# Performance work log

Measured on AMD Instinct MI355X. Metric: run time of the kernel, lower is better.

The kernel has to match this reference:

```python
import jax, jax.numpy as jnp
import numpy as np

SMOOTHING = 0.05
CONFIDENCE = 1.0 - SMOOTHING
B, C = 32768, 2048


def setup_inputs() -> dict:
    key = jax.random.key(0)
    k1, k2, k3 = jax.random.split(key, 3)
    x = jax.random.normal(k1, (B, C), dtype=jnp.float32)
    target = jax.random.randint(k2, (B,), 0, C, dtype=jnp.int64)
    class_loss_weight = jax.random.uniform(k3, (C,), dtype=jnp.float32)
    return {"x": x, "target": target, "class_loss_weight": class_loss_weight}


def reference(x, target, class_loss_weight):
    # logprobs: [B, C]
    logprobs = jax.nn.log_softmax(x, axis=-1)
    # nll_loss: [B] = -logprobs[i, target[i]]
    nll_loss = -jnp.take_along_axis(logprobs, target[:, None], axis=-1)[:, 0]
    # smooth_loss: [B] = -mean over classes
    smooth_loss = -jnp.mean(logprobs, axis=-1)
    # per-sample class weights (vectorized replacement for the python loop)
    w = class_loss_weight[target]  # [B]
    w_sum = jnp.sum(w)
    loss = CONFIDENCE * nll_loss * w + SMOOTHING * smooth_loss
    return jnp.sum(loss) / w_sum
```

## Files before the change

### kernel.cpp

```cpp
#include <hip/hip_runtime.h>
#include <math.h>

#define SMOOTHING_F   0.05f
#define CONFIDENCE_F  0.95f
#define C_DIM         2048

#define STAGE1_BLOCKS 128

__global__ __launch_bounds__(256) void ls_main(
    const float* __restrict__ x,
    const int*   __restrict__ target,
    const float* __restrict__ cw,
    double*      __restrict__ ws)
{
    const int row  = blockIdx.x;
    const int tid  = threadIdx.x;
    const int lane = tid & 63;
    const int wave = tid >> 6;

    const int t = target[row];

    const float4* xr = (const float4*)(x + (size_t)row * C_DIM);
    const float4 a = xr[tid];
    const float4 b = xr[tid + 256];

    const float wt = cw[t];
    const float xt = x[(size_t)row * C_DIM + t];

    float se = __expf(a.x) + __expf(a.y) + __expf(a.z) + __expf(a.w)
             + __expf(b.x) + __expf(b.y) + __expf(b.z) + __expf(b.w);
    float sx = (a.x + a.y) + (a.z + a.w) + (b.x + b.y) + (b.z + b.w);

#pragma unroll
    for (int off = 32; off > 0; off >>= 1) {
        se += __shfl_xor(se, off, 64);
        sx += __shfl_xor(sx, off, 64);
    }

    __shared__ float sSe[4], sSx[4];
    if (lane == 0) { sSe[wave] = se; sSx[wave] = sx; }
    __syncthreads();
    if (tid == 0) {
        const float seT = (sSe[0] + sSe[1]) + (sSe[2] + sSe[3]);
        const float sxT = (sSx[0] + sSx[1]) + (sSx[2] + sSx[3]);
        const float lse = __logf(seT);
        const float nll    = lse - xt;
        const float smooth = lse - sxT * (1.0f / C_DIM);
        const double loss = (double)(CONFIDENCE_F * nll * wt + SMOOTHING_F * smooth);
        ws[2 * (size_t)row]     = loss;
        ws[2 * (size_t)row + 1] = (double)wt;
    }
}

__global__ __launch_bounds__(256) void ls_reduce1(
    const double* __restrict__ ws, double* __restrict__ out1, int B)
{
    const int tid  = threadIdx.x;
    const int lane = tid & 63;
    const int wave = tid >> 6;

    double L = 0.0, W = 0.0;
    for (int i = blockIdx.x * 256 + tid; i < B; i += STAGE1_BLOCKS * 256) {
        L += ws[2 * (size_t)i];
        W += ws[2 * (size_t)i + 1];
    }
#pragma unroll
    for (int off = 32; off > 0; off >>= 1) {
        L += __shfl_xor(L, off, 64);
        W += __shfl_xor(W, off, 64);
    }
    __shared__ double sL[4], sW[4];
    if (lane == 0) { sL[wave] = L; sW[wave] = W; }
    __syncthreads();
    if (tid == 0) {
        out1[2 * blockIdx.x]     = (sL[0] + sL[1]) + (sL[2] + sL[3]);
        out1[2 * blockIdx.x + 1] = (sW[0] + sW[1]) + (sW[2] + sW[3]);
    }
}

__global__ __launch_bounds__(128) void ls_reduce2(
    const double* __restrict__ in1, float* __restrict__ out)
{
    const int tid  = threadIdx.x;
    const int lane = tid & 63;
    const int wave = tid >> 6;

    double L = in1[2 * tid];
    double W = in1[2 * tid + 1];
#pragma unroll
    for (int off = 32; off > 0; off >>= 1) {
        L += __shfl_xor(L, off, 64);
        W += __shfl_xor(W, off, 64);
    }
    __shared__ double sL[2], sW[2];
    if (lane == 0) { sL[wave] = L; sW[wave] = W; }
    __syncthreads();
    if (tid == 0) out[0] = (float)((sL[0] + sL[1]) / (sW[0] + sW[1]));
}

extern "C" void kernel_launch(void* const* d_in, const int* in_sizes, int n_in,
                              void* d_out, int out_size, void* d_ws, size_t ws_size,
                              hipStream_t stream) {
    const float* x      = (const float*)d_in[0];
    const int*   target = (const int*)  d_in[1];
    const float* cw     = (const float*)d_in[2];
    float*       out    = (float*)d_out;
    double*      ws     = (double*)d_ws;

    const int B = in_sizes[1];
    double* stage1 = ws + 2 * (size_t)B;

    ls_main<<<B, 256, 0, stream>>>(x, target, cw, ws);
    ls_reduce1<<<STAGE1_BLOCKS, 256, 0, stream>>>(ws, stage1, B);
    ls_reduce2<<<1, 128, 0, stream>>>(stage1, out);
}
```

Baseline: 351.1 us.

## Use nontemporal loads/stores and collapse two-stage reduction into one kernel

The main kernel now loads x with nontemporal loads, writes each row's loss and weight pair as a single nontemporal 16-byte store, and declares a launch-bounds occupancy hint. The two-kernel reduction is replaced by one 1024-thread single-block kernel that reads the paired partials as vectors. This removes one kernel launch and its inter-kernel gap, at the cost of the final reduction running on a single CU over 32K pairs.

```diff
diff --git a/kernel.cpp b/kernel.cpp
--- a/kernel.cpp
+++ b/kernel.cpp
@@ -5,9 +5,10 @@
 #define CONFIDENCE_F  0.95f
 #define C_DIM         2048
 
-#define STAGE1_BLOCKS 128
+typedef float  f32x4 __attribute__((ext_vector_type(4)));
+typedef double f64x2 __attribute__((ext_vector_type(2)));
 
-__global__ __launch_bounds__(256) void ls_main(
+__global__ __launch_bounds__(256, 8) void ls_main(
     const float* __restrict__ x,
     const int*   __restrict__ target,
     const float* __restrict__ cw,
@@ -20,9 +21,9 @@
 
     const int t = target[row];
 
-    const float4* xr = (const float4*)(x + (size_t)row * C_DIM);
-    const float4 a = xr[tid];
-    const float4 b = xr[tid + 256];
+    const f32x4* xr = (const f32x4*)(x + (size_t)row * C_DIM);
+    const f32x4 a = __builtin_nontemporal_load(&xr[tid]);
+    const f32x4 b = __builtin_nontemporal_load(&xr[tid + 256]);
 
     const float wt = cw[t];
     const float xt = x[(size_t)row * C_DIM + t];
@@ -46,56 +47,40 @@
         const float lse = __logf(seT);
         const float nll    = lse - xt;
         const float smooth = lse - sxT * (1.0f / C_DIM);
-        const double loss = (double)(CONFIDENCE_F * nll * wt + SMOOTHING_F * smooth);
-        ws[2 * (size_t)row]     = loss;
-        ws[2 * (size_t)row + 1] = (double)wt;
+        f64x2 part;
+        part.x = (double)(CONFIDENCE_F * nll * wt + SMOOTHING_F * smooth);
+        part.y = (double)wt;
+        __builtin_nontemporal_store(part, (f64x2*)ws + row);
     }
 }
 
-__global__ __launch_bounds__(256) void ls_reduce1(
-    const double* __restrict__ ws, double* __restrict__ out1, int B)
+__global__ __launch_bounds__(1024) void ls_reduce(
+    const double* __restrict__ ws, float* __restrict__ out, int B)
 {
     const int tid  = threadIdx.x;
     const int lane = tid & 63;
     const int wave = tid >> 6;
 
+    const f64x2* p = (const f64x2*)ws;
     double L = 0.0, W = 0.0;
-    for (int i = blockIdx.x * 256 + tid; i < B; i += STAGE1_BLOCKS * 256) {
-        L += ws[2 * (size_t)i];
-        W += ws[2 * (size_t)i + 1];
+    for (int i = tid; i < B; i += 1024) {
+        const f64x2 v = p[i];
+        L += v.x; W += v.y;
     }
 #pragma unroll
     for (int off = 32; off > 0; off >>= 1) {
         L += __shfl_xor(L, off, 64);
         W += __shfl_xor(W, off, 64);
     }
-    __shared__ double sL[4], sW[4];
+    __shared__ double sL[16], sW[16];
     if (lane == 0) { sL[wave] = L; sW[wave] = W; }
     __syncthreads();
     if (tid == 0) {
-        out1[2 * blockIdx.x]     = (sL[0] + sL[1]) + (sL[2] + sL[3]);
-        out1[2 * blockIdx.x + 1] = (sW[0] + sW[1]) + (sW[2] + sW[3]);
+        double tL = 0.0, tW = 0.0;
+#pragma unroll
+        for (int i = 0; i < 16; ++i) { tL += sL[i]; tW += sW[i]; }
+        out[0] = (float)(tL / tW);
     }
-}
-
-__global__ __launch_bounds__(128) void ls_reduce2(
-    const double* __restrict__ in1, float* __restrict__ out)
-{
-    const int tid  = threadIdx.x;
-    const int lane = tid & 63;
-    const int wave = tid >> 6;
-
-    double L = in1[2 * tid];
-    double W = in1[2 * tid + 1];
-#pragma unroll
-    for (int off = 32; off > 0; off >>= 1) {
-        L += __shfl_xor(L, off, 64);
-        W += __shfl_xor(W, off, 64);
-    }
-    __shared__ double sL[2], sW[2];
-    if (lane == 0) { sL[wave] = L; sW[wave] = W; }
-    __syncthreads();
-    if (tid == 0) out[0] = (float)((sL[0] + sL[1]) / (sW[0] + sW[1]));
 }
 
 extern "C" void kernel_launch(void* const* d_in, const int* in_sizes, int n_in,
@@ -108,9 +93,7 @@
     double*      ws     = (double*)d_ws;
 
     const int B = in_sizes[1];
-    double* stage1 = ws + 2 * (size_t)B;
 
     ls_main<<<B, 256, 0, stream>>>(x, target, cw, ws);
-    ls_reduce1<<<STAGE1_BLOCKS, 256, 0, stream>>>(ws, stage1, B);
-    ls_reduce2<<<1, 128, 0, stream>>>(stage1, out);
+    ls_reduce<<<1, 1024, 0, stream>>>(ws, out, B);
 }
```

Result: no change. 356.0 us (+1.4%).
